# Performance work log

Hardware: AMD Instinct MI355X
Metric: run time of the kernel (lower is better)

## Reference

```python
import jax, jax.numpy as jnp
import numpy as np

B, T, H = 16, 2048, 1024
L_ORDER, R_ORDER = 1, 1
K = L_ORDER + R_ORDER + 1
THRESH = 1.0


def _alphas(hidden, conv_w, conv_b, lin_w, lin_b):
    # hidden: [B, T, H]
    context = jnp.swapaxes(hidden, 1, 2)  # [B, H, T]
    q = jnp.pad(context, ((0, 0), (0, 0), (L_ORDER, R_ORDER)))  # ConstantPad1d
    mem = jax.lax.conv_general_dilated(
        q, conv_w, (1,), 'VALID',
        dimension_numbers=('NCH', 'OIH', 'NCH'),
        feature_group_count=conv_w.shape[0])  # depthwise conv, groups=idim
    mem = mem + conv_b[None, :, None]
    out = jnp.swapaxes(mem + context, 1, 2)  # [B, T, H] (dropout = identity, eval)
    out = jax.nn.relu(out)
    out = out @ lin_w.T + lin_b  # [B, T, 1]
    return jax.nn.sigmoid(out)[..., 0]  # [B, T]


def _cif_scan(hidden, alphas, threshold):
    # sequential integrate-and-fire over time, vectorized over batch via lax.scan
    b, t, h = hidden.shape

    def step(carry, xs):
        integrate, frame = carry          # [B], [B, H]
        alpha, h_t = xs                   # [B], [B, H]
        dist = 1.0 - integrate            # distribution_completion
        integrate = integrate + alpha
        fires_t = integrate
        fire = integrate >= threshold
        integrate = jnp.where(fire, integrate - 1.0, integrate)
        cur = jnp.where(fire, dist, alpha)
        rem = alpha - cur
        frame = frame + cur[:, None] * h_t
        frames_t = frame
        frame = jnp.where(fire[:, None], rem[:, None] * h_t, frame)
        return (integrate, frame), (fires_t, frames_t)

    init = (jnp.zeros((b,), hidden.dtype), jnp.zeros((b, h), hidden.dtype))
    xs = (jnp.swapaxes(alphas, 0, 1), jnp.swapaxes(hidden, 0, 1))
    _, (fires, frames) = jax.lax.scan(step, init, xs)
    return jnp.swapaxes(frames, 0, 1), jnp.swapaxes(fires, 0, 1)  # [B,T,H], [B,T]


def _gather_fired(frames, fires, threshold, max_label_len):
    # per-batch select frames where fires>=threshold, pad to max_label_len
    b, t, h = frames.shape
    mask = fires >= threshold                         # [B, T]
    rank = jnp.cumsum(mask.astype(jnp.int32), axis=1) - 1
    idx = jnp.where(mask, rank, max_label_len)        # invalid -> dummy row
    out = jnp.zeros((b, max_label_len + 1, h), frames.dtype)
    out = out.at[jnp.arange(b)[:, None], idx].add(
        jnp.where(mask[..., None], frames, 0.0))
    return out[:, :max_label_len]


def setup_inputs() -> dict:
    key = jax.random.key(0)
    k1, k2, k3, k4 = jax.random.split(key, 4)
    hidden = jax.random.normal(k1, (B, T, H), jnp.float32)
    conv_w = jax.random.normal(k2, (H, 1, K), jnp.float32) / np.sqrt(K)
    conv_b = jax.random.normal(k3, (H,), jnp.float32) * 0.01
    lin_w = jax.random.normal(k4, (1, H), jnp.float32) / np.sqrt(H)
    lin_b = jnp.zeros((1,), jnp.float32)
    return {"hidden": hidden, "conv_w": conv_w, "conv_b": conv_b,
            "lin_w": lin_w, "lin_b": lin_b}


def reference(hidden, conv_w, conv_b, lin_w, lin_b):
    alphas = _alphas(hidden, conv_w, conv_b, lin_w, lin_b)  # [B, T]
    cif_length = alphas.sum(-1)                             # [B]
    frames, fires = _cif_scan(hidden, alphas, THRESH)
    # data-dependent output length (matches torch: round(alphas.sum(-1)).max())
    max_label_len = int(jnp.round(cif_length).astype(jnp.int32).max())
    cif_output = _gather_fired(frames, fires, THRESH, max_label_len)
    return cif_output, cif_length, fires
```

## Files before the change

### kernel.cpp

```cpp
#include <hip/hip_runtime.h>
#include <math.h>

#define B_ 16
#define T_ 2048
#define H_ 1024
#define TPB 16

__global__ __launch_bounds__(256) void k1_alphas(
    const float* __restrict__ hidden, const float* __restrict__ conv_w,
    const float* __restrict__ conv_b, const float* __restrict__ lin_w,
    const float* __restrict__ lin_b, float* __restrict__ alphas)
{
    const int tile = blockIdx.x & (T_ / TPB - 1);
    const int b    = blockIdx.x / (T_ / TPB);
    const int tid  = threadIdx.x;
    const int h0   = tid * 4;

    float w0[4], w1[4], w2[4];
    {
        const float4* cw = (const float4*)(conv_w + (size_t)h0 * 3);
        float4 c0 = cw[0], c1 = cw[1], c2 = cw[2];
        w0[0] = c0.x; w1[0] = c0.y; w2[0] = c0.z;
        w0[1] = c0.w; w1[1] = c1.x; w2[1] = c1.y;
        w0[2] = c1.z; w1[2] = c1.w; w2[2] = c2.x;
        w0[3] = c2.y; w1[3] = c2.z; w2[3] = c2.w;
    }
    const float4 cb = *(const float4*)(conv_b + h0);
    const float4 lw = *(const float4*)(lin_w + h0);
    const float  lb = lin_b[0];

    const size_t base = ((size_t)b * T_) * H_ + h0;
    const int t0 = tile * TPB;

    float4 prev = (t0 > 0) ? *(const float4*)(hidden + base + (size_t)(t0 - 1) * H_)
                           : make_float4(0.f, 0.f, 0.f, 0.f);
    float4 curr = *(const float4*)(hidden + base + (size_t)t0 * H_);
    float4 next;

    __shared__ float lds[4][TPB];
    const int wave = tid >> 6;
    const int lane = tid & 63;

    #pragma unroll
    for (int tt = 0; tt < TPB; ++tt) {
        const int t = t0 + tt;
        next = (t + 1 < T_) ? *(const float4*)(hidden + base + (size_t)(t + 1) * H_)
                            : make_float4(0.f, 0.f, 0.f, 0.f);
        float p = 0.f, v;
        v = fmaf(w0[0], prev.x, fmaf(w1[0], curr.x, fmaf(w2[0], next.x, cb.x + curr.x)));
        p = fmaf(fmaxf(v, 0.f), lw.x, p);
        v = fmaf(w0[1], prev.y, fmaf(w1[1], curr.y, fmaf(w2[1], next.y, cb.y + curr.y)));
        p = fmaf(fmaxf(v, 0.f), lw.y, p);
        v = fmaf(w0[2], prev.z, fmaf(w1[2], curr.z, fmaf(w2[2], next.z, cb.z + curr.z)));
        p = fmaf(fmaxf(v, 0.f), lw.z, p);
        v = fmaf(w0[3], prev.w, fmaf(w1[3], curr.w, fmaf(w2[3], next.w, cb.w + curr.w)));
        p = fmaf(fmaxf(v, 0.f), lw.w, p);
        #pragma unroll
        for (int m = 32; m; m >>= 1) p += __shfl_xor(p, m);
        if (lane == 0) lds[wave][tt] = p;
        prev = curr; curr = next;
    }
    __syncthreads();
    if (tid < TPB) {
        float s = lds[0][tid] + lds[1][tid] + lds[2][tid] + lds[3][tid] + lb;
        alphas[(size_t)b * T_ + t0 + tid] = 1.f / (1.f + expf(-s));
    }
}

__global__ __launch_bounds__(64) void k2a_scan(
    const float* __restrict__ alphas, float* __restrict__ fires)
{
    const int b = threadIdx.x;
    if (b >= B_) return;
    const float* a = alphas + (size_t)b * T_;
    float* f = fires + (size_t)b * T_;
    float I = 0.f;
    float4 c0 = *(const float4*)(a);
    float4 c1 = *(const float4*)(a + 4);
    float4 n0 = make_float4(0, 0, 0, 0), n1 = n0;
    for (int t = 0; t < T_; t += 8) {
        if (t + 8 < T_) {
            n0 = *(const float4*)(a + t + 8);
            n1 = *(const float4*)(a + t + 12);
        }
        float av[8] = {c0.x, c0.y, c0.z, c0.w, c1.x, c1.y, c1.z, c1.w};
        float fv[8];
        #pragma unroll
        for (int j = 0; j < 8; ++j) {
            I += av[j];
            fv[j] = I;
            I = __builtin_amdgcn_fractf(I);
        }
        *(float4*)(f + t)     = make_float4(fv[0], fv[1], fv[2], fv[3]);
        *(float4*)(f + t + 4) = make_float4(fv[4], fv[5], fv[6], fv[7]);
        c0 = n0; c1 = n1;
    }
}

__global__ __launch_bounds__(256) void k2b_coef(
    const float* __restrict__ alphas, const float* __restrict__ fires,
    float* __restrict__ cur, float* __restrict__ rem,
    int* __restrict__ fire_pos, int* __restrict__ n_fires,
    float* __restrict__ cif_length, int Lpad)
{
    const int b = blockIdx.x;
    const int tid = threadIdx.x;
    const int t0 = tid * 8;
    const size_t base = (size_t)b * T_;

    float a[8], f[8];
    *(float4*)(a)     = *(const float4*)(alphas + base + t0);
    *(float4*)(a + 4) = *(const float4*)(alphas + base + t0 + 4);
    *(float4*)(f)     = *(const float4*)(fires + base + t0);
    *(float4*)(f + 4) = *(const float4*)(fires + base + t0 + 4);
    const float fprev = (t0 == 0) ? 0.f : fires[base + t0 - 1];

    float cu[8], re[8];
    bool fr[8];
    float asum = 0.f;
    int cnt = 0;
    #pragma unroll
    for (int j = 0; j < 8; ++j) {
        float fp = (j == 0) ? fprev : f[j - 1];
        float Iprev = __builtin_amdgcn_fractf(fp);
        fr[j] = (f[j] >= 1.f);
        const float dist = 1.f - Iprev;
        cu[j] = fr[j] ? dist : a[j];
        re[j] = a[j] - cu[j];
        cnt += fr[j] ? 1 : 0;
        asum += a[j];
    }
    *(float4*)(cur + base + t0)     = *(float4*)(cu);
    *(float4*)(cur + base + t0 + 4) = *(float4*)(cu + 4);
    *(float4*)(rem + base + t0)     = *(float4*)(re);
    *(float4*)(rem + base + t0 + 4) = *(float4*)(re + 4);

    const int lane = tid & 63, wave = tid >> 6;
    int inc = cnt;
    #pragma unroll
    for (int d = 1; d < 64; d <<= 1) {
        int v = __shfl_up(inc, d);
        if (lane >= d) inc += v;
    }
    __shared__ int wsum[4];
    if (lane == 63) wsum[wave] = inc;
    __syncthreads();
    int waveoff = 0;
    for (int w = 0; w < wave; ++w) waveoff += wsum[w];
    int r = waveoff + inc - cnt;
    #pragma unroll
    for (int j = 0; j < 8; ++j) {
        if (fr[j]) {
            if (r < Lpad) fire_pos[b * Lpad + r] = t0 + j;
            ++r;
        }
    }
    if (tid == 255) n_fires[b] = waveoff + inc;

    float s = asum;
    #pragma unroll
    for (int m = 32; m; m >>= 1) s += __shfl_xor(s, m);
    __shared__ float wred[4];
    if (lane == 0) wred[wave] = s;
    __syncthreads();
    if (tid == 0) cif_length[b] = wred[0] + wred[1] + wred[2] + wred[3];
}

__global__ __launch_bounds__(256) void k3_frames(
    const float* __restrict__ hidden, const float* __restrict__ cur,
    const float* __restrict__ rem, const int* __restrict__ fire_pos,
    const int* __restrict__ n_fires, float* __restrict__ out,
    int L, int Lpad)
{
    const int k = blockIdx.x;
    const int b = blockIdx.y;
    const int tid = threadIdx.x;
    const int h0 = tid * 4;
    float4 acc = make_float4(0.f, 0.f, 0.f, 0.f);
    const int n = n_fires[b];
    if (k < n) {
        const int e = fire_pos[b * Lpad + k];
        const int s = (k > 0) ? fire_pos[b * Lpad + k - 1] : -1;
        const size_t hb = ((size_t)b * T_) * H_ + h0;
        if (k > 0) {
            const float w = rem[(size_t)b * T_ + s];
            const float4 hr = *(const float4*)(hidden + hb + (size_t)s * H_);
            acc.x = w * hr.x; acc.y = w * hr.y; acc.z = w * hr.z; acc.w = w * hr.w;
        }
        for (int t = s + 1; t <= e; ++t) {
            const float w = cur[(size_t)b * T_ + t];
            const float4 hr = *(const float4*)(hidden + hb + (size_t)t * H_);
            acc.x = fmaf(w, hr.x, acc.x); acc.y = fmaf(w, hr.y, acc.y);
            acc.z = fmaf(w, hr.z, acc.z); acc.w = fmaf(w, hr.w, acc.w);
        }
    }
    *(float4*)(out + ((size_t)b * L + k) * H_ + h0) = acc;
}

extern "C" void kernel_launch(void* const* d_in, const int* in_sizes, int n_in,
                              void* d_out, int out_size, void* d_ws, size_t ws_size,
                              hipStream_t stream) {
    const float* hidden = (const float*)d_in[0];
    const float* conv_w = (const float*)d_in[1];
    const float* conv_b = (const float*)d_in[2];
    const float* lin_w  = (const float*)d_in[3];
    const float* lin_b  = (const float*)d_in[4];
    float* out = (float*)d_out;

    const int L = (out_size - B_ - B_ * T_) / (B_ * H_);
    float* cif_output = out;
    float* cif_length = out + (size_t)B_ * L * H_;
    float* fires      = cif_length + B_;

    float* alphas = (float*)d_ws;
    float* cur    = alphas + (size_t)B_ * T_;
    float* rem    = cur + (size_t)B_ * T_;
    const int Lpad = L + 8;
    int* fire_pos = (int*)(rem + (size_t)B_ * T_);
    int* n_fires  = fire_pos + (size_t)B_ * Lpad;

    k1_alphas<<<dim3(B_ * (T_ / TPB)), 256, 0, stream>>>(
        hidden, conv_w, conv_b, lin_w, lin_b, alphas);
    k2a_scan<<<dim3(1), 64, 0, stream>>>(alphas, fires);
    k2b_coef<<<dim3(B_), 256, 0, stream>>>(
        alphas, fires, cur, rem, fire_pos, n_fires, cif_length, Lpad);
    k3_frames<<<dim3(L, B_), 256, 0, stream>>>(
        hidden, cur, rem, fire_pos, n_fires, cif_output, L, Lpad);
}
```

Measured before the change: 278.2 us.

## Fuse scan into coefficient kernel and process several frames per block

Merges the sequential fire scan into the coefficient kernel, so each batch row runs its scan serially in LDS inside a 16-block launch instead of as a separate single-block kernel. This removes one launch and the global round trip for fires. The frames kernel now handles KPB consecutive output frames per block and reuses the boundary hidden row across frames, avoiding a reload of the fire-boundary row. The trade-off is a serial single-thread scan per block over LDS and fewer blocks in the frames kernel, which lowers parallelism.

```diff
diff --git a/kernel.cpp b/kernel.cpp
--- a/kernel.cpp
+++ b/kernel.cpp
@@ -5,6 +5,7 @@
 #define T_ 2048
 #define H_ 1024
 #define TPB 16
+#define KPB 8
 
 __global__ __launch_bounds__(256) void k1_alphas(
     const float* __restrict__ hidden, const float* __restrict__ conv_w,
@@ -67,53 +68,47 @@
     }
 }
 
-__global__ __launch_bounds__(64) void k2a_scan(
-    const float* __restrict__ alphas, float* __restrict__ fires)
-{
-    const int b = threadIdx.x;
-    if (b >= B_) return;
-    const float* a = alphas + (size_t)b * T_;
-    float* f = fires + (size_t)b * T_;
-    float I = 0.f;
-    float4 c0 = *(const float4*)(a);
-    float4 c1 = *(const float4*)(a + 4);
-    float4 n0 = make_float4(0, 0, 0, 0), n1 = n0;
-    for (int t = 0; t < T_; t += 8) {
-        if (t + 8 < T_) {
-            n0 = *(const float4*)(a + t + 8);
-            n1 = *(const float4*)(a + t + 12);
-        }
-        float av[8] = {c0.x, c0.y, c0.z, c0.w, c1.x, c1.y, c1.z, c1.w};
-        float fv[8];
-        #pragma unroll
-        for (int j = 0; j < 8; ++j) {
-            I += av[j];
-            fv[j] = I;
-            I = __builtin_amdgcn_fractf(I);
-        }
-        *(float4*)(f + t)     = make_float4(fv[0], fv[1], fv[2], fv[3]);
-        *(float4*)(f + t + 4) = make_float4(fv[4], fv[5], fv[6], fv[7]);
-        c0 = n0; c1 = n1;
-    }
-}
-
-__global__ __launch_bounds__(256) void k2b_coef(
-    const float* __restrict__ alphas, const float* __restrict__ fires,
+__global__ __launch_bounds__(256) void k2_scan_coef(
+    const float* __restrict__ alphas, float* __restrict__ fires,
     float* __restrict__ cur, float* __restrict__ rem,
     int* __restrict__ fire_pos, int* __restrict__ n_fires,
     float* __restrict__ cif_length, int Lpad)
 {
     const int b = blockIdx.x;
     const int tid = threadIdx.x;
+    const size_t base = (size_t)b * T_;
+
+    __shared__ float sA[T_];
+    __shared__ float sF[T_];
+
+    {
+        const int i = tid * 8;
+        *(float4*)(sA + i)     = *(const float4*)(alphas + base + i);
+        *(float4*)(sA + i + 4) = *(const float4*)(alphas + base + i + 4);
+    }
+    __syncthreads();
+
+    if (tid == 0) {
+        float I = 0.f;
+        for (int t = 0; t < T_; t += 8) {
+            #pragma unroll
+            for (int j = 0; j < 8; ++j) {
+                I += sA[t + j];
+                sF[t + j] = I;
+                I = __builtin_amdgcn_fractf(I);
+            }
+        }
+    }
+    __syncthreads();
+
     const int t0 = tid * 8;
-    const size_t base = (size_t)b * T_;
-
     float a[8], f[8];
-    *(float4*)(a)     = *(const float4*)(alphas + base + t0);
-    *(float4*)(a + 4) = *(const float4*)(alphas + base + t0 + 4);
-    *(float4*)(f)     = *(const float4*)(fires + base + t0);
-    *(float4*)(f + 4) = *(const float4*)(fires + base + t0 + 4);
-    const float fprev = (t0 == 0) ? 0.f : fires[base + t0 - 1];
+    #pragma unroll
+    for (int j = 0; j < 8; ++j) { a[j] = sA[t0 + j]; f[j] = sF[t0 + j]; }
+    const float fprev = (t0 == 0) ? 0.f : sF[t0 - 1];
+
+    *(float4*)(fires + base + t0)     = make_float4(f[0], f[1], f[2], f[3]);
+    *(float4*)(fires + base + t0 + 4) = make_float4(f[4], f[5], f[6], f[7]);
 
     float cu[8], re[8];
     bool fr[8];
@@ -172,29 +167,51 @@
     const int* __restrict__ n_fires, float* __restrict__ out,
     int L, int Lpad)
 {
-    const int k = blockIdx.x;
-    const int b = blockIdx.y;
+    const int k0 = blockIdx.x * KPB;
+    const int b  = blockIdx.y;
     const int tid = threadIdx.x;
     const int h0 = tid * 4;
-    float4 acc = make_float4(0.f, 0.f, 0.f, 0.f);
     const int n = n_fires[b];
-    if (k < n) {
-        const int e = fire_pos[b * Lpad + k];
-        const int s = (k > 0) ? fire_pos[b * Lpad + k - 1] : -1;
-        const size_t hb = ((size_t)b * T_) * H_ + h0;
-        if (k > 0) {
-            const float w = rem[(size_t)b * T_ + s];
-            const float4 hr = *(const float4*)(hidden + hb + (size_t)s * H_);
-            acc.x = w * hr.x; acc.y = w * hr.y; acc.z = w * hr.z; acc.w = w * hr.w;
+    const size_t hb = ((size_t)b * T_) * H_ + h0;
+    const size_t cb = (size_t)b * T_;
+
+    int s = -1;
+    float4 hprev = make_float4(0.f, 0.f, 0.f, 0.f);
+    if (k0 > 0) {
+        s = fire_pos[b * Lpad + k0 - 1];
+        if (k0 < n)
+            hprev = *(const float4*)(hidden + hb + (size_t)s * H_);
+    }
+
+    #pragma unroll 1
+    for (int kk = 0; kk < KPB; ++kk) {
+        const int k = k0 + kk;
+        if (k >= L) break;
+        float4 acc = make_float4(0.f, 0.f, 0.f, 0.f);
+        if (k < n) {
+            const int e = fire_pos[b * Lpad + k];
+            if (k > 0) {
+                const float w = rem[cb + s];
+                acc.x = w * hprev.x; acc.y = w * hprev.y;
+                acc.z = w * hprev.z; acc.w = w * hprev.w;
+            }
+            for (int t = s + 1; t < e; ++t) {
+                const float w = cur[cb + t];
+                const float4 hr = *(const float4*)(hidden + hb + (size_t)t * H_);
+                acc.x = fmaf(w, hr.x, acc.x); acc.y = fmaf(w, hr.y, acc.y);
+                acc.z = fmaf(w, hr.z, acc.z); acc.w = fmaf(w, hr.w, acc.w);
+            }
+            {
+                const float w = cur[cb + e];
+                const float4 hr = *(const float4*)(hidden + hb + (size_t)e * H_);
+                acc.x = fmaf(w, hr.x, acc.x); acc.y = fmaf(w, hr.y, acc.y);
+                acc.z = fmaf(w, hr.z, acc.z); acc.w = fmaf(w, hr.w, acc.w);
+                hprev = hr;
+            }
+            s = e;
         }
-        for (int t = s + 1; t <= e; ++t) {
-            const float w = cur[(size_t)b * T_ + t];
-            const float4 hr = *(const float4*)(hidden + hb + (size_t)t * H_);
-            acc.x = fmaf(w, hr.x, acc.x); acc.y = fmaf(w, hr.y, acc.y);
-            acc.z = fmaf(w, hr.z, acc.z); acc.w = fmaf(w, hr.w, acc.w);
-        }
-    }
-    *(float4*)(out + ((size_t)b * L + k) * H_ + h0) = acc;
+        *(float4*)(out + ((size_t)b * L + k) * H_ + h0) = acc;
+    }
 }
 
 extern "C" void kernel_launch(void* const* d_in, const int* in_sizes, int n_in,
@@ -221,9 +238,8 @@
 
     k1_alphas<<<dim3(B_ * (T_ / TPB)), 256, 0, stream>>>(
         hidden, conv_w, conv_b, lin_w, lin_b, alphas);
-    k2a_scan<<<dim3(1), 64, 0, stream>>>(alphas, fires);
-    k2b_coef<<<dim3(B_), 256, 0, stream>>>(
+    k2_scan_coef<<<dim3(B_), 256, 0, stream>>>(
         alphas, fires, cur, rem, fire_pos, n_fires, cif_length, Lpad);
-    k3_frames<<<dim3(L, B_), 256, 0, stream>>>(
+    k3_frames<<<dim3((L + KPB - 1) / KPB, B_), 256, 0, stream>>>(
         hidden, cur, rem, fire_pos, n_fires, cif_output, L, Lpad);
 }
```

After: 262.4 us. 1.06x faster.
